# Kernel optimization log

Measured on AMD Instinct MI355X. Metric: run time of the kernel, lower is better.

The kernel has to match this reference:

```python
import jax, jax.numpy as jnp
import numpy as np

EMBED_DIM = 1024
NUM_HEADS = 16
HEAD_DIM = EMBED_DIM // NUM_HEADS


def setup_inputs() -> dict:
    key = jax.random.key(0)
    ks = jax.random.split(key, 9)
    B, T, C = 2, 2048, EMBED_DIM
    s = 1.0 / np.sqrt(C)
    inp = {
        "x": jax.random.normal(ks[0], (B, T, C), dtype=jnp.float32),
        "Wq": jax.random.uniform(ks[1], (C, C), jnp.float32, -s, s),
        "bq": jax.random.uniform(ks[2], (C,), jnp.float32, -s, s),
        "Wk": jax.random.uniform(ks[3], (C, C), jnp.float32, -s, s),
        "bk": jax.random.uniform(ks[4], (C,), jnp.float32, -s, s),
        "Wv": jax.random.uniform(ks[5], (C, C), jnp.float32, -s, s),
        "bv": jax.random.uniform(ks[6], (C,), jnp.float32, -s, s),
        "Wo": jax.random.uniform(ks[7], (C, C), jnp.float32, -s, s),
        "bo": jax.random.uniform(ks[8], (C,), jnp.float32, -s, s),
    }
    return inp


def reference(x, Wq, bq, Wk, bk, Wv, bv, Wo, bo):
    B, T, C = x.shape
    H, D = NUM_HEADS, HEAD_DIM

    def heads(W, b):
        # [B,T,C] -> [B,H,T,D]
        return (x @ W + b).reshape(B, T, H, D).transpose(0, 2, 1, 3)

    q = heads(Wq, bq)
    k = heads(Wk, bk)
    v = heads(Wv, bv)

    scores = jnp.einsum('bhtd,bhsd->bhts', q, k) / np.sqrt(D).astype(np.float32)
    causal = jnp.tril(jnp.ones((T, T), dtype=bool))  # [T,T]
    scores = jnp.where(causal[None, None], scores, -jnp.inf)
    weights = jax.nn.softmax(scores, axis=-1)
    out = jnp.einsum('bhts,bhsd->bhtd', weights, v)  # [B,H,T,D]
    out = out.transpose(0, 2, 1, 3).reshape(B, T, C)
    return out @ Wo + bo
```

## Files before the change

### kernel.cpp

```cpp
#include <hip/hip_runtime.h>
#include <stdint.h>

#define T_LEN 2048
#define C_DIM 1024
#define NHEAD 16
#define HDIM  64
#define MTOT  4096

typedef __bf16 bf16;
typedef __bf16 bf16x8 __attribute__((ext_vector_type(8)));
typedef float  f32x4  __attribute__((ext_vector_type(4)));

__device__ __forceinline__ bf16 f2bf(float f) {
    union { float f; unsigned u; } x; x.f = f;
    unsigned r = x.u + 0x7fffu + ((x.u >> 16) & 1u);
    unsigned short h = (unsigned short)(r >> 16);
    return __builtin_bit_cast(bf16, h);
}

__device__ __forceinline__ void g2l16(const void* g, const void* l) {
    __builtin_amdgcn_global_load_lds(
        (const __attribute__((address_space(1))) unsigned int*)(uintptr_t)g,
        (__attribute__((address_space(3))) unsigned int*)(uint32_t)(uintptr_t)l,
        16, 0, 0);
}


__global__ void cast_x_kernel(const float* __restrict__ x, bf16* __restrict__ xb) {
    int f = blockIdx.x * 256 + threadIdx.x;
    const float4* p = (const float4*)x + (size_t)f * 2;
    float4 a = p[0], b = p[1];
    bf16x8 o;
    o[0] = f2bf(a.x); o[1] = f2bf(a.y); o[2] = f2bf(a.z); o[3] = f2bf(a.w);
    o[4] = f2bf(b.x); o[5] = f2bf(b.y); o[6] = f2bf(b.z); o[7] = f2bf(b.w);
    ((bf16x8*)xb)[f] = o;
}

__global__ void cast_w_kernel(const float* __restrict__ W0, const float* __restrict__ W1,
                              const float* __restrict__ W2, const float* __restrict__ W3,
                              bf16* __restrict__ wt) {
    __shared__ float tile[64][68];
    const int tid = threadIdx.x;
    const int w = blockIdx.z;
    const float* W = (w == 0) ? W0 : (w == 1) ? W1 : (w == 2) ? W2 : W3;
    const int kb = blockIdx.x * 64, nb = blockIdx.y * 64;
#pragma unroll
    for (int pass = 0; pass < 4; ++pass) {
        int row = pass * 16 + (tid >> 4);
        int col = (tid & 15) * 4;
        float4 v = *(const float4*)(W + (size_t)(kb + row) * 1024 + nb + col);
        *(float4*)(&tile[row][col]) = v;
    }
    __syncthreads();
#pragma unroll
    for (int pass = 0; pass < 2; ++pass) {
        int s = pass * 256 + tid;
        int nn = s >> 3, c = s & 7;
        bf16x8 o;
#pragma unroll
        for (int j = 0; j < 8; ++j) o[j] = f2bf(tile[c * 8 + j][nn]);
        *(bf16x8*)(wt + (size_t)w * 1048576 + (size_t)(nb + nn) * 1024 + kb + c * 8) = o;
    }
}

__global__ void transpose_v_kernel(const bf16* __restrict__ V, bf16* __restrict__ Vtp) {
    __shared__ bf16 tile[128][72];
    const int tid = threadIdx.x;
    const int t0 = blockIdx.x * 128, bh = blockIdx.y;
    const size_t hb = (size_t)bh * 131072;
#pragma unroll
    for (int pass = 0; pass < 4; ++pass) {
        int s = pass * 256 + tid;
        int row = s >> 3, c = s & 7;
        bf16x8 v = *(const bf16x8*)(V + hb + (size_t)(t0 + row) * 64 + c * 8);
        *(bf16x8*)(&tile[row][c * 8]) = v;
    }
    __syncthreads();
#pragma unroll
    for (int pass = 0; pass < 4; ++pass) {
        int s = pass * 256 + tid;
        int d = s >> 4, ch = s & 15;
        bf16x8 o;
#pragma unroll
        for (int j = 0; j < 8; ++j) o[j] = tile[j * 16 + ch][d];
        *(bf16x8*)(Vtp + hb + (size_t)d * 2048 + t0 + ch * 8) = o;
    }
}

__global__ __launch_bounds__(256, 2)
void gemm_bt_kernel(const bf16* __restrict__ A, const bf16* __restrict__ WtAll,
                    const float* __restrict__ b0, const float* __restrict__ b1,
                    const float* __restrict__ b2, bf16* __restrict__ outQKV) {
    __shared__ char lds[32768];
    bf16* As = (bf16*)lds;
    bf16* Bs = (bf16*)(lds + 16384);

    const int tid = threadIdx.x;
    const int lane = tid & 63, wid = tid >> 6;
    const int r = lane & 15, q4 = lane >> 4;
    const int mbase = blockIdx.y * 128;
    const int nbase = blockIdx.x * 128;
    const int z = blockIdx.z;
    const bf16* Bt = WtAll + (size_t)z * 1048576;
    const float* bias = (z == 0) ? b0 : (z == 1) ? b1 : b2;
    const float osc = (z == 0) ? 0.125f : 1.0f;

    const int wm = (wid >> 1) * 64;
    const int wn = (wid & 1) * 64;

    float bv[4];
#pragma unroll
    for (int j = 0; j < 4; ++j) bv[j] = bias[nbase + wn + j * 16 + r];

    f32x4 acc[4][4];
#pragma unroll
    for (int i = 0; i < 4; ++i)
#pragma unroll
        for (int j = 0; j < 4; ++j) acc[i][j] = f32x4{0.f, 0.f, 0.f, 0.f};

    for (int kt = 0; kt < 16; ++kt) {
        int kb = kt * 64;
#pragma unroll
        for (int p = 0; p < 4; ++p) {
            int s = p * 256 + tid;
            int row = s >> 3, blk = s & 7;
            int sb = blk ^ (row & 7);
            g2l16(A  + (size_t)(mbase + row) * 1024 + kb + sb * 8, (char*)As + s * 16);
            g2l16(Bt + (size_t)(nbase + row) * 1024 + kb + sb * 8, (char*)Bs + s * 16);
        }
        __syncthreads();
#pragma unroll
        for (int ks = 0; ks < 2; ++ks) {
            int blk = ks * 4 + q4;
            bf16x8 a[4], b[4];
#pragma unroll
            for (int i = 0; i < 4; ++i) {
                int rowa = wm + i * 16 + r;
                a[i] = *(const bf16x8*)((const char*)As + rowa * 128 + ((blk ^ (rowa & 7)) * 16));
                int rowb = wn + i * 16 + r;
                b[i] = *(const bf16x8*)((const char*)Bs + rowb * 128 + ((blk ^ (rowb & 7)) * 16));
            }
#pragma unroll
            for (int i = 0; i < 4; ++i)
#pragma unroll
                for (int j = 0; j < 4; ++j)
                    acc[i][j] = __builtin_amdgcn_mfma_f32_16x16x32_bf16(a[i], b[j], acc[i][j], 0, 0, 0);
        }
        __syncthreads();
    }

#pragma unroll
    for (int i = 0; i < 4; ++i) {
        int m0 = mbase + wm + i * 16 + q4 * 4;
#pragma unroll
        for (int j = 0; j < 4; ++j) {
            int n = nbase + wn + j * 16 + r;
#pragma unroll
            for (int reg = 0; reg < 4; ++reg) {
                float v = (acc[i][j][reg] + bv[j]) * osc;
                int mm = m0 + reg;
                int bi = mm >> 11, t = mm & 2047, h = n >> 6, d = n & 63;
                outQKV[(size_t)z * 4194304 + ((size_t)(bi * 16 + h) * 2048 + t) * 64 + d] = f2bf(v);
            }
        }
    }
}

__global__ __launch_bounds__(256, 2)
void gemm_o_kernel(const bf16* __restrict__ A, const bf16* __restrict__ Bt,
                   const float* __restrict__ bias, float* __restrict__ out) {
    __shared__ char lds[24576];
    bf16* As = (bf16*)lds;
    bf16* Bs = (bf16*)(lds + 16384);

    const int tid = threadIdx.x;
    const int lane = tid & 63, wid = tid >> 6;
    const int r = lane & 15, q4 = lane >> 4;
    const int nb = blockIdx.x * 64;
    const int mb = blockIdx.y * 128;
    const int wm = (wid >> 1) * 64;
    const int wn = (wid & 1) * 32;

    float bv[2];
#pragma unroll
    for (int j = 0; j < 2; ++j) bv[j] = bias[nb + wn + j * 16 + r];

    f32x4 acc[4][2];
#pragma unroll
    for (int i = 0; i < 4; ++i)
#pragma unroll
        for (int j = 0; j < 2; ++j) acc[i][j] = f32x4{0.f, 0.f, 0.f, 0.f};

    for (int kt = 0; kt < 16; ++kt) {
        int kb = kt * 64;
#pragma unroll
        for (int p = 0; p < 4; ++p) {
            int s = p * 256 + tid;
            int row = s >> 3, blk = s & 7;
            g2l16(A + (size_t)(mb + row) * 1024 + kb + ((blk ^ (row & 7)) * 8), (char*)As + s * 16);
        }
#pragma unroll
        for (int p = 0; p < 2; ++p) {
            int s = p * 256 + tid;
            int row = s >> 3, blk = s & 7;
            g2l16(Bt + (size_t)(nb + row) * 1024 + kb + ((blk ^ (row & 7)) * 8), (char*)Bs + s * 16);
        }
        __syncthreads();
#pragma unroll
        for (int ks = 0; ks < 2; ++ks) {
            int blk = ks * 4 + q4;
            bf16x8 a[4], b[2];
#pragma unroll
            for (int i = 0; i < 4; ++i) {
                int rowa = wm + i * 16 + r;
                a[i] = *(const bf16x8*)((const char*)As + rowa * 128 + ((blk ^ (rowa & 7)) * 16));
            }
#pragma unroll
            for (int j = 0; j < 2; ++j) {
                int rowb = wn + j * 16 + r;
                b[j] = *(const bf16x8*)((const char*)Bs + rowb * 128 + ((blk ^ (rowb & 7)) * 16));
            }
#pragma unroll
            for (int i = 0; i < 4; ++i)
#pragma unroll
                for (int j = 0; j < 2; ++j)
                    acc[i][j] = __builtin_amdgcn_mfma_f32_16x16x32_bf16(a[i], b[j], acc[i][j], 0, 0, 0);
        }
        __syncthreads();
    }

#pragma unroll
    for (int i = 0; i < 4; ++i) {
        int m0 = mb + wm + i * 16 + q4 * 4;
#pragma unroll
        for (int j = 0; j < 2; ++j) {
            int n = nb + wn + j * 16 + r;
#pragma unroll
            for (int reg = 0; reg < 4; ++reg)
                out[(size_t)(m0 + reg) * 1024 + n] = acc[i][j][reg] + bv[j];
        }
    }
}

__global__ __launch_bounds__(256, 2)
void attn_kernel(const bf16* __restrict__ Q, const bf16* __restrict__ K,
                 const bf16* __restrict__ Vtp, bf16* __restrict__ Aout) {
    __shared__ char lds[49152];
    bf16* Ks = (bf16*)lds;
    bf16* Vs = (bf16*)(lds + 16384);
    bf16* Ps = (bf16*)(lds + 32768);

    const int tid = threadIdx.x, lane = tid & 63, wid = tid >> 6;
    const int r = lane & 15, q4 = lane >> 4;
    const int p = blockIdx.x >> 5;
    const int bh = blockIdx.x & 31;
    const int b = bh >> 4, h = bh & 15;
    const size_t hb = (size_t)bh * 131072;
    bf16* Pw = Ps + wid * 2048;

    for (int phase = 0; phase < 2; ++phase) {
        const int qi = phase ? (31 - p) : p;
        const int qbase = qi * 64;
        const int qrow = qbase + wid * 16 + r;

        bf16x8 qf[2];
        qf[0] = *(const bf16x8*)(Q + hb + (size_t)qrow * 64 + q4 * 8);
        qf[1] = *(const bf16x8*)(Q + hb + (size_t)qrow * 64 + 32 + q4 * 8);

        f32x4 o[4];
        float lip[4];
#pragma unroll
        for (int jd = 0; jd < 4; ++jd) o[jd] = f32x4{0.f, 0.f, 0.f, 0.f};
#pragma unroll
        for (int reg = 0; reg < 4; ++reg) lip[reg] = 0.f;

        const int ntiles = (qi >> 1) + 1;
        for (int kt = 0; kt < ntiles; ++kt) {
            int kb = kt * 128;
#pragma unroll
            for (int pp = 0; pp < 4; ++pp) {
                int s = pp * 256 + tid;
                int row = s >> 3, blk = s & 7;
                g2l16(K + hb + (size_t)(kb + row) * 64 + ((blk ^ (row & 7)) * 8), (char*)Ks + s * 16);
            }
#pragma unroll
            for (int pp = 0; pp < 4; ++pp) {
                int s = pp * 256 + tid;
                int row = s >> 4, ch = s & 15;
                g2l16(Vtp + hb + (size_t)row * 2048 + kb + ((ch ^ (row & 15)) * 8), (char*)Vs + s * 16);
            }
            __syncthreads();

            f32x4 sc[8];
#pragma unroll
            for (int jn = 0; jn < 8; ++jn) {
                int rowk = jn * 16 + r;
                bf16x8 bk0 = *(const bf16x8*)((const char*)Ks + rowk * 128 + ((q4 ^ (rowk & 7)) * 16));
                bf16x8 bk1 = *(const bf16x8*)((const char*)Ks + rowk * 128 + (((4 + q4) ^ (rowk & 7)) * 16));
                sc[jn] = __builtin_amdgcn_mfma_f32_16x16x32_bf16(qf[0], bk0, f32x4{0.f, 0.f, 0.f, 0.f}, 0, 0, 0);
                sc[jn] = __builtin_amdgcn_mfma_f32_16x16x32_bf16(qf[1], bk1, sc[jn], 0, 0, 0);
            }

            const bool lastt = (kt == ntiles - 1);
#pragma unroll
            for (int reg = 0; reg < 4; ++reg) {
                int rowl = q4 * 4 + reg;
                int grow = qbase + wid * 16 + rowl;
                bf16x8 pp8;
                float rs = 0.f;
                if (lastt) {
#pragma unroll
                    for (int jn = 0; jn < 8; ++jn) {
                        float sv = (kb + jn * 16 + r > grow) ? -1e30f : sc[jn][reg];
                        float pv = __expf(sv);
                        rs += pv;
                        pp8[jn] = (bf16)pv;
                    }
                } else {
#pragma unroll
                    for (int jn = 0; jn < 8; ++jn) {
                        float pv = __expf(sc[jn][reg]);
                        rs += pv;
                        pp8[jn] = (bf16)pv;
                    }
                }
                lip[reg] += rs;
                *(bf16x8*)((char*)Pw + rowl * 256 + ((r ^ rowl) * 16)) = pp8;
            }

#pragma unroll
            for (int s4 = 0; s4 < 4; ++s4) {
                int c = s4 * 4 + q4;
                bf16x8 ap = *(const bf16x8*)((const char*)Pw + r * 256 + ((c ^ r) * 16));
#pragma unroll
                for (int jd = 0; jd < 4; ++jd) {
                    int rowd = jd * 16 + r;
                    bf16x8 bv8 = *(const bf16x8*)((const char*)Vs + rowd * 256 + ((c ^ (rowd & 15)) * 16));
                    o[jd] = __builtin_amdgcn_mfma_f32_16x16x32_bf16(ap, bv8, o[jd], 0, 0, 0);
                }
            }
            __syncthreads();
        }

#pragma unroll
        for (int reg = 0; reg < 4; ++reg) {
            float li = lip[reg];
            li += __shfl_xor(li, 1);
            li += __shfl_xor(li, 2);
            li += __shfl_xor(li, 4);
            li += __shfl_xor(li, 8);
            float inv = 1.f / li;
            int grow = qbase + wid * 16 + q4 * 4 + reg;
#pragma unroll
            for (int jd = 0; jd < 4; ++jd) {
                int d = jd * 16 + r;
                Aout[((size_t)(b * 2048 + grow)) * 1024 + h * 64 + d] = f2bf(o[jd][reg] * inv);
            }
        }
    }
}


extern "C" void kernel_launch(void* const* d_in, const int* in_sizes, int n_in,
                              void* d_out, int out_size, void* d_ws, size_t ws_size,
                              hipStream_t stream) {
    const float* x  = (const float*)d_in[0];
    const float* Wq = (const float*)d_in[1];
    const float* bq = (const float*)d_in[2];
    const float* Wk = (const float*)d_in[3];
    const float* bk = (const float*)d_in[4];
    const float* Wv = (const float*)d_in[5];
    const float* bv = (const float*)d_in[6];
    const float* Wo = (const float*)d_in[7];
    const float* bo = (const float*)d_in[8];
    float* out = (float*)d_out;

    char* ws = (char*)d_ws;
    bf16* xb   = (bf16*)(ws);
    bf16* wt   = (bf16*)(ws + 8388608);
    bf16* qkv  = (bf16*)(ws + 16777216);
    bf16* vtp  = (bf16*)(ws + 41943040);
    bf16* attn = (bf16*)(ws + 50331648);

    hipLaunchKernelGGL(cast_x_kernel, dim3(2048), dim3(256), 0, stream, x, xb);
    hipLaunchKernelGGL(cast_w_kernel, dim3(16, 16, 4), dim3(256), 0, stream, Wq, Wk, Wv, Wo, wt);
    hipLaunchKernelGGL(gemm_bt_kernel, dim3(8, 32, 3), dim3(256), 0, stream,
                       xb, wt, bq, bk, bv, qkv);
    hipLaunchKernelGGL(transpose_v_kernel, dim3(16, 32), dim3(256), 0, stream,
                       qkv + (size_t)2 * 4194304, vtp);
    hipLaunchKernelGGL(attn_kernel, dim3(512), dim3(256), 0, stream,
                       qkv, qkv + 4194304, vtp, attn);
    hipLaunchKernelGGL(gemm_o_kernel, dim3(16, 32), dim3(256), 0, stream,
                       attn, wt + (size_t)3 * 1048576, bo, out);
}
```

Baseline: 171.9 us.

## Double-buffer K/V tiles and process 128-row query blocks per attention wave

The attention kernel now gives each wave 32 query rows instead of 16 and uses 128-row query tiles. Blocks are paired as p and 15-p to balance causal work, and the grid is halved to 256. K/V tiles are double-buffered in 96KB of LDS, so the next tile's global-to-LDS load is issued while the current one is computed, which removes one barrier per iteration. Each LDS-loaded K/V fragment now feeds twice as many MFMAs. The cost is higher register pressure, occupancy of one block per CU, and fewer blocks than CUs. The QKV GEMM launch bound is also raised to 3 blocks per CU.

```diff
diff --git a/kernel.cpp b/kernel.cpp
--- a/kernel.cpp
+++ b/kernel.cpp
@@ -87,7 +87,7 @@
     }
 }
 
-__global__ __launch_bounds__(256, 2)
+__global__ __launch_bounds__(256, 3)
 void gemm_bt_kernel(const bf16* __restrict__ A, const bf16* __restrict__ WtAll,
                     const float* __restrict__ b0, const float* __restrict__ b1,
                     const float* __restrict__ b2, bf16* __restrict__ outQKV) {
@@ -242,13 +242,10 @@
     }
 }
 
-__global__ __launch_bounds__(256, 2)
+__global__ __launch_bounds__(256, 1)
 void attn_kernel(const bf16* __restrict__ Q, const bf16* __restrict__ K,
                  const bf16* __restrict__ Vtp, bf16* __restrict__ Aout) {
-    __shared__ char lds[49152];
-    bf16* Ks = (bf16*)lds;
-    bf16* Vs = (bf16*)(lds + 16384);
-    bf16* Ps = (bf16*)(lds + 32768);
+    __shared__ char lds[98304];
 
     const int tid = threadIdx.x, lane = tid & 63, wid = tid >> 6;
     const int r = lane & 15, q4 = lane >> 4;
@@ -256,62 +253,122 @@
     const int bh = blockIdx.x & 31;
     const int b = bh >> 4, h = bh & 15;
     const size_t hb = (size_t)bh * 131072;
-    bf16* Pw = Ps + wid * 2048;
-
-    for (int phase = 0; phase < 2; ++phase) {
-        const int qi = phase ? (31 - p) : p;
-        const int qbase = qi * 64;
-        const int qrow = qbase + wid * 16 + r;
-
-        bf16x8 qf[2];
-        qf[0] = *(const bf16x8*)(Q + hb + (size_t)qrow * 64 + q4 * 8);
-        qf[1] = *(const bf16x8*)(Q + hb + (size_t)qrow * 64 + 32 + q4 * 8);
-
-        f32x4 o[4];
-        float lip[4];
-#pragma unroll
-        for (int jd = 0; jd < 4; ++jd) o[jd] = f32x4{0.f, 0.f, 0.f, 0.f};
-#pragma unroll
-        for (int reg = 0; reg < 4; ++reg) lip[reg] = 0.f;
-
-        const int ntiles = (qi >> 1) + 1;
-        for (int kt = 0; kt < ntiles; ++kt) {
-            int kb = kt * 128;
-#pragma unroll
-            for (int pp = 0; pp < 4; ++pp) {
-                int s = pp * 256 + tid;
-                int row = s >> 3, blk = s & 7;
-                g2l16(K + hb + (size_t)(kb + row) * 64 + ((blk ^ (row & 7)) * 8), (char*)Ks + s * 16);
-            }
-#pragma unroll
-            for (int pp = 0; pp < 4; ++pp) {
-                int s = pp * 256 + tid;
-                int row = s >> 4, ch = s & 15;
-                g2l16(Vtp + hb + (size_t)row * 2048 + kb + ((ch ^ (row & 15)) * 8), (char*)Vs + s * 16);
-            }
-            __syncthreads();
-
-            f32x4 sc[8];
-#pragma unroll
-            for (int jn = 0; jn < 8; ++jn) {
-                int rowk = jn * 16 + r;
-                bf16x8 bk0 = *(const bf16x8*)((const char*)Ks + rowk * 128 + ((q4 ^ (rowk & 7)) * 16));
-                bf16x8 bk1 = *(const bf16x8*)((const char*)Ks + rowk * 128 + (((4 + q4) ^ (rowk & 7)) * 16));
-                sc[jn] = __builtin_amdgcn_mfma_f32_16x16x32_bf16(qf[0], bk0, f32x4{0.f, 0.f, 0.f, 0.f}, 0, 0, 0);
-                sc[jn] = __builtin_amdgcn_mfma_f32_16x16x32_bf16(qf[1], bk1, sc[jn], 0, 0, 0);
-            }
-
-            const bool lastt = (kt == ntiles - 1);
+    char* Pw = lds + 65536 + wid * 8192;
+
+    const int qiA = p, qiB = 15 - p;
+    const int itB0 = qiA + 1;
+    const int ittot = itB0 + qiB + 1;
+
+    bf16x8 qfA[2][2], qfB[2][2], qf[2][2];
+#pragma unroll
+    for (int i = 0; i < 2; ++i)
+#pragma unroll
+        for (int ks = 0; ks < 2; ++ks) {
+            int rA = qiA * 128 + wid * 32 + i * 16 + r;
+            int rB = qiB * 128 + wid * 32 + i * 16 + r;
+            qfA[i][ks] = *(const bf16x8*)(Q + hb + (size_t)rA * 64 + ks * 32 + q4 * 8);
+            qfB[i][ks] = *(const bf16x8*)(Q + hb + (size_t)rB * 64 + ks * 32 + q4 * 8);
+            qf[i][ks] = qfA[i][ks];
+        }
+
+    f32x4 o[2][4];
+    float lip[2][4];
+#pragma unroll
+    for (int i = 0; i < 2; ++i)
+#pragma unroll
+        for (int jd = 0; jd < 4; ++jd) { o[i][jd] = f32x4{0.f, 0.f, 0.f, 0.f}; lip[i][jd] = 0.f; }
+
+    auto stage = [&](int buf, int kb) {
+        char* Kb = lds + buf * 16384;
+        char* Vb = lds + 32768 + buf * 16384;
+#pragma unroll
+        for (int pp = 0; pp < 4; ++pp) {
+            int s = pp * 256 + tid;
+            int row = s >> 3, blk = s & 7;
+            g2l16(K + hb + (size_t)(kb + row) * 64 + ((blk ^ (row & 7)) * 8), Kb + s * 16);
+        }
+#pragma unroll
+        for (int pp = 0; pp < 4; ++pp) {
+            int s = pp * 256 + tid;
+            int row = s >> 4, ch = s & 15;
+            g2l16(Vtp + hb + (size_t)row * 2048 + kb + ((ch ^ (row & 15)) * 8), Vb + s * 16);
+        }
+    };
+
+    auto epilogue = [&](int qbase) {
+#pragma unroll
+        for (int i = 0; i < 2; ++i)
 #pragma unroll
             for (int reg = 0; reg < 4; ++reg) {
-                int rowl = q4 * 4 + reg;
-                int grow = qbase + wid * 16 + rowl;
+                float li = lip[i][reg];
+                li += __shfl_xor(li, 1);
+                li += __shfl_xor(li, 2);
+                li += __shfl_xor(li, 4);
+                li += __shfl_xor(li, 8);
+                float inv = 1.f / li;
+                int grow = qbase + wid * 32 + i * 16 + q4 * 4 + reg;
+#pragma unroll
+                for (int jd = 0; jd < 4; ++jd) {
+                    int d = jd * 16 + r;
+                    Aout[((size_t)(b * 2048 + grow)) * 1024 + h * 64 + d] = f2bf(o[i][jd][reg] * inv);
+                }
+            }
+    };
+
+    stage(0, 0);
+
+    for (int it = 0; it < ittot; ++it) {
+        __syncthreads();
+        const int cb = it & 1;
+        if (it + 1 < ittot) {
+            int nit = it + 1;
+            int nkt = (nit < itB0) ? nit : (nit - itB0);
+            stage(nit & 1, nkt * 128);
+        }
+        if (it == itB0) {
+            epilogue(qiA * 128);
+#pragma unroll
+            for (int i = 0; i < 2; ++i) {
+#pragma unroll
+                for (int jd = 0; jd < 4; ++jd) { o[i][jd] = f32x4{0.f, 0.f, 0.f, 0.f}; lip[i][jd] = 0.f; }
+#pragma unroll
+                for (int ks = 0; ks < 2; ++ks) qf[i][ks] = qfB[i][ks];
+            }
+        }
+        const bool inB = (it >= itB0);
+        const int qi = inB ? qiB : qiA;
+        const int kt = inB ? (it - itB0) : it;
+        const int kb = kt * 128;
+        const int qbase = qi * 128;
+        const char* Kb = lds + cb * 16384;
+        const char* Vb = lds + 32768 + cb * 16384;
+
+        f32x4 sc[2][8];
+#pragma unroll
+        for (int jn = 0; jn < 8; ++jn) {
+            int rowk = jn * 16 + r;
+            bf16x8 bk0 = *(const bf16x8*)(Kb + rowk * 128 + ((q4 ^ (rowk & 7)) * 16));
+            bf16x8 bk1 = *(const bf16x8*)(Kb + rowk * 128 + (((4 + q4) ^ (rowk & 7)) * 16));
+#pragma unroll
+            for (int i = 0; i < 2; ++i) {
+                sc[i][jn] = __builtin_amdgcn_mfma_f32_16x16x32_bf16(qf[i][0], bk0, f32x4{0.f, 0.f, 0.f, 0.f}, 0, 0, 0);
+                sc[i][jn] = __builtin_amdgcn_mfma_f32_16x16x32_bf16(qf[i][1], bk1, sc[i][jn], 0, 0, 0);
+            }
+        }
+
+        const bool lastt = (kt == qi);
+#pragma unroll
+        for (int i = 0; i < 2; ++i) {
+#pragma unroll
+            for (int reg = 0; reg < 4; ++reg) {
+                int rowl = i * 16 + q4 * 4 + reg;
+                int grow = qbase + wid * 32 + rowl;
                 bf16x8 pp8;
                 float rs = 0.f;
                 if (lastt) {
 #pragma unroll
                     for (int jn = 0; jn < 8; ++jn) {
-                        float sv = (kb + jn * 16 + r > grow) ? -1e30f : sc[jn][reg];
+                        float sv = (kb + jn * 16 + r > grow) ? -1e30f : sc[i][jn][reg];
                         float pv = __expf(sv);
                         rs += pv;
                         pp8[jn] = (bf16)pv;
@@ -319,45 +376,32 @@
                 } else {
 #pragma unroll
                     for (int jn = 0; jn < 8; ++jn) {
-                        float pv = __expf(sc[jn][reg]);
+                        float pv = __expf(sc[i][jn][reg]);
                         rs += pv;
                         pp8[jn] = (bf16)pv;
                     }
                 }
-                lip[reg] += rs;
-                *(bf16x8*)((char*)Pw + rowl * 256 + ((r ^ rowl) * 16)) = pp8;
-            }
-
-#pragma unroll
-            for (int s4 = 0; s4 < 4; ++s4) {
-                int c = s4 * 4 + q4;
-                bf16x8 ap = *(const bf16x8*)((const char*)Pw + r * 256 + ((c ^ r) * 16));
-#pragma unroll
-                for (int jd = 0; jd < 4; ++jd) {
-                    int rowd = jd * 16 + r;
-                    bf16x8 bv8 = *(const bf16x8*)((const char*)Vs + rowd * 256 + ((c ^ (rowd & 15)) * 16));
-                    o[jd] = __builtin_amdgcn_mfma_f32_16x16x32_bf16(ap, bv8, o[jd], 0, 0, 0);
-                }
-            }
-            __syncthreads();
-        }
-
-#pragma unroll
-        for (int reg = 0; reg < 4; ++reg) {
-            float li = lip[reg];
-            li += __shfl_xor(li, 1);
-            li += __shfl_xor(li, 2);
-            li += __shfl_xor(li, 4);
-            li += __shfl_xor(li, 8);
-            float inv = 1.f / li;
-            int grow = qbase + wid * 16 + q4 * 4 + reg;
+                lip[i][reg] += rs;
+                *(bf16x8*)(Pw + rowl * 256 + ((r ^ (rowl & 15)) * 16)) = pp8;
+            }
+        }
+
+#pragma unroll
+        for (int s4 = 0; s4 < 4; ++s4) {
+            int c = s4 * 4 + q4;
+            bf16x8 ap0 = *(const bf16x8*)(Pw + r * 256 + ((c ^ r) * 16));
+            bf16x8 ap1 = *(const bf16x8*)(Pw + (16 + r) * 256 + ((c ^ r) * 16));
 #pragma unroll
             for (int jd = 0; jd < 4; ++jd) {
-                int d = jd * 16 + r;
-                Aout[((size_t)(b * 2048 + grow)) * 1024 + h * 64 + d] = f2bf(o[jd][reg] * inv);
-            }
-        }
-    }
+                int rowd = jd * 16 + r;
+                bf16x8 bv8 = *(const bf16x8*)(Vb + rowd * 256 + ((c ^ (rowd & 15)) * 16));
+                o[0][jd] = __builtin_amdgcn_mfma_f32_16x16x32_bf16(ap0, bv8, o[0][jd], 0, 0, 0);
+                o[1][jd] = __builtin_amdgcn_mfma_f32_16x16x32_bf16(ap1, bv8, o[1][jd], 0, 0, 0);
+            }
+        }
+    }
+
+    epilogue(qiB * 128);
 }
 
 
@@ -388,7 +432,7 @@
                        xb, wt, bq, bk, bv, qkv);
     hipLaunchKernelGGL(transpose_v_kernel, dim3(16, 32), dim3(256), 0, stream,
                        qkv + (size_t)2 * 4194304, vtp);
-    hipLaunchKernelGGL(attn_kernel, dim3(512), dim3(256), 0, stream,
+    hipLaunchKernelGGL(attn_kernel, dim3(256), dim3(256), 0, stream,
                        qkv, qkv + 4194304, vtp, attn);
     hipLaunchKernelGGL(gemm_o_kernel, dim3(16, 32), dim3(256), 0, stream,
                        attn, wt + (size_t)3 * 1048576, bo, out);
```

After: 184.9 us. 1.08x slower.
